# Kernel optimization log

Measured on AMD Instinct MI355X. Metric: run time of the kernel, lower is better.

## Reference

```python
import jax, jax.numpy as jnp
import numpy as np

INPUT_H = 512
INPUT_W = 512
POOL = 5
BN_EPS = 1e-5


def setup_inputs() -> dict:
    key = jax.random.key(0)
    ks = jax.random.split(key, 8)
    B = 16
    c3 = jax.random.normal(ks[0], (B, 512, 64, 64), jnp.float32)
    c4 = jax.random.normal(ks[1], (B, 1024, 32, 32), jnp.float32)
    xy = jax.random.uniform(ks[2], (B, 10, 4), jnp.float32) * 512.0
    # ensure x1<=x2, y1<=y2 like real detector boxes
    boxes = jnp.concatenate([jnp.minimum(xy[..., :2], xy[..., 2:]),
                             jnp.maximum(xy[..., :2], xy[..., 2:])], axis=-1)
    w_conv = jax.random.normal(ks[3], (512, 1536), jnp.float32) * 0.02  # 1x1 conv kernel
    b_conv = jnp.zeros((512,), jnp.float32)
    bn_gamma = jnp.ones((512,), jnp.float32)
    bn_beta = jnp.zeros((512,), jnp.float32)
    bn_mean = jax.random.normal(ks[4], (512,), jnp.float32) * 0.1
    bn_var = jax.random.uniform(ks[5], (512,), jnp.float32) * 0.5 + 0.5
    return {"c3": c3, "c4": c4, "boxes": boxes, "w_conv": w_conv, "b_conv": b_conv,
            "bn_gamma": bn_gamma, "bn_beta": bn_beta, "bn_mean": bn_mean, "bn_var": bn_var}


def _bin_weights(lo, hi, size, nout):
    """Adaptive-avg-pool bin weights over axis of length `size` for crop [lo,hi).
    Returns [nout, size] row-stochastic matrix (same math as AdaptiveAvgPool1d bins)."""
    length = hi - lo
    k = jnp.arange(nout)
    starts = lo + (k * length) // nout                      # floor(k*L/n)
    ends = lo + ((k + 1) * length + nout - 1) // nout        # ceil((k+1)*L/n)
    idx = jnp.arange(size)
    mask = (idx[None, :] >= starts[:, None]) & (idx[None, :] < ends[:, None])
    return mask.astype(jnp.float32) / (ends - starts)[:, None].astype(jnp.float32)


def reference(c3, c4, boxes, w_conv, b_conv, bn_gamma, bn_beta, bn_mean, bn_var):
    B = c3.shape[0]
    c4u = jax.image.resize(c4, (B, c4.shape[1], c4.shape[2] * 2, c4.shape[3] * 2),
                           method='bilinear')
    fused = jnp.concatenate([c3, c4u], axis=1)               # [B,1536,H,W]
    y = jnp.einsum('bchw,oc->bohw', fused, w_conv) + b_conv[None, :, None, None]
    inv = bn_gamma / jnp.sqrt(bn_var + BN_EPS)               # eval-mode BN
    y = y * inv[None, :, None, None] + (bn_beta - bn_mean * inv)[None, :, None, None]
    attr_blob = jax.nn.relu(y)                               # [B,512,H,W]
    H, W = attr_blob.shape[-2:]
    sx = W / INPUT_W
    sy = H / INPUT_H

    def pool_one(feat, box):  # feat [C,H,W], box [4] -> [C,5,5]
        x1 = jnp.clip(jnp.floor(box[0] * sx), 0, W - 1).astype(jnp.int32)
        y1 = jnp.clip(jnp.floor(box[1] * sy), 0, H - 1).astype(jnp.int32)
        x2 = jnp.clip(jnp.ceil(box[2] * sx), 0, W - 1).astype(jnp.int32)
        y2 = jnp.clip(jnp.ceil(box[3] * sy), 0, H - 1).astype(jnp.int32)
        x2 = jnp.where(x2 <= x1, jnp.minimum(x1 + 1, W), x2)
        y2 = jnp.where(y2 <= y1, jnp.minimum(y1 + 1, H), y2)
        wy = _bin_weights(y1, y2, H, POOL)                   # [5,H]
        wx = _bin_weights(x1, x2, W, POOL)                   # [5,W]
        return jnp.einsum('ph,chw,qw->cpq', wy, feat, wx)

    obj_blob = jax.vmap(lambda f, bx: jax.vmap(lambda b: pool_one(f, b))(bx))(attr_blob, boxes)
    return boxes, obj_blob  # ([B,10,4], [B,10,512,5,5])
```

## Files before the change

kernel.cpp:

```cpp
#include <hip/hip_runtime.h>
#include <stdint.h>

#define FH 64
#define FW 64
#define CIN 1536
#define C3C 512
#define C4C 1024
#define COUT 512
#define BATCH 16
#define NPIX 4096
#define NBOX 10
#define MPAD 256
#define KT128 12

typedef float v4f __attribute__((ext_vector_type(4)));
typedef long  v2l __attribute__((ext_vector_type(2)));

#define GLOAD_LDS16(g, l) __builtin_amdgcn_global_load_lds( \
    (const __attribute__((address_space(1))) void*)(g),     \
    (__attribute__((address_space(3))) void*)(l), 16, 0, 0)

#define BARRIER() asm volatile("s_barrier" ::: "memory")

__device__ __forceinline__ uint32_t pack4_fp8(float a, float b, float c, float d) {
    int lo = __builtin_amdgcn_cvt_pk_fp8_f32(a, b, 0, false);
    int v  = __builtin_amdgcn_cvt_pk_fp8_f32(c, d, lo, true);
    return (uint32_t)v;
}
__device__ __forceinline__ unsigned char f32_to_fp8(float a) {
    return (unsigned char)(__builtin_amdgcn_cvt_pk_fp8_f32(a, a, 0, false) & 0xff);
}


__global__ void prep_bn(const float* __restrict__ bng, const float* __restrict__ bnb,
                        const float* __restrict__ bnm, const float* __restrict__ bnv,
                        const float* __restrict__ bconv,
                        float* __restrict__ scale, float* __restrict__ shift) {
    int o = threadIdx.x;
    if (o < COUT) {
        float inv = bng[o] / sqrtf(bnv[o] + 1e-5f);
        scale[o] = inv * 0.0625f;
        shift[o] = bnb[o] + inv * (bconv[o] - bnm[o]);
    }
}

__global__ void conv_w(const float* __restrict__ w, unsigned char* __restrict__ w8, int n4) {
    int i = blockIdx.x * 256 + threadIdx.x;
    if (i < n4) {
        float4 f = *(const float4*)(w + i * 4);
        uint32_t v = pack4_fp8(f.x * 16.0f, f.y * 16.0f, f.z * 16.0f, f.w * 16.0f);
        int c0 = (i * 4) % CIN;
        int o  = (i * 4) / CIN;
        int k7 = c0 & 127;
        int pos = ((k7 >> 3) & 3) * 32 + (k7 >> 5) * 8 + (k7 & 7);
        *(uint32_t*)(w8 + (size_t)o * CIN + (c0 & ~127) + pos) = v;
    }
}

__global__ __launch_bounds__(256) void build_fusedT(const float* __restrict__ c3,
                                                    const float* __restrict__ c4,
                                                    unsigned char* __restrict__ fusedT) {
    __shared__ uint32_t lds[64 * 36];
    int ct = blockIdx.x;
    int y  = blockIdx.y;
    int b  = blockIdx.z;
    int t  = threadIdx.x;
    int pg = t & 15;
    int cq = t >> 4;

    #pragma unroll
    for (int r = 0; r < 2; ++r) {
        int cquad = cq + 16 * r;
        float vv[4][4];
        if (ct < 4) {
            int ch = ct * 128 + 4 * cquad;
            const float* src = c3 + (((size_t)(b * C3C + ch) * FH + y) * FW) + 4 * pg;
            #pragma unroll
            for (int k = 0; k < 4; ++k) {
                float4 f = *(const float4*)(src + (size_t)k * (FH * FW));
                vv[k][0] = f.x; vv[k][1] = f.y; vv[k][2] = f.z; vv[k][3] = f.w;
            }
        } else {
            int ch = ct * 128 - 512 + 4 * cquad;
            int jy = y >> 1;
            int jyB = min(max(jy + ((y & 1) ? 1 : -1), 0), 31);
            const float* base = c4 + (size_t)(b * C4C + ch) * 1024;
            #pragma unroll
            for (int k = 0; k < 4; ++k) {
                const float* pc = base + (size_t)k * 1024;
                float2 f0 = *(const float2*)(pc + jy * 32 + 2 * pg);
                float2 f1 = *(const float2*)(pc + jyB * 32 + 2 * pg);
                float rbA = 0.75f * f0.x + 0.25f * f1.x;
                float rbB = 0.75f * f0.y + 0.25f * f1.y;
                float rbm = __shfl_up(rbB, 1, 16);
                float rbp = __shfl_down(rbA, 1, 16);
                if (pg == 0)  rbm = rbA;
                if (pg == 15) rbp = rbB;
                vv[k][0] = 0.75f * rbA + 0.25f * rbm;
                vv[k][1] = 0.75f * rbA + 0.25f * rbB;
                vv[k][2] = 0.75f * rbB + 0.25f * rbA;
                vv[k][3] = 0.75f * rbB + 0.25f * rbp;
            }
        }
        #pragma unroll
        for (int i = 0; i < 4; ++i) {
            int px = 4 * pg + i;
            lds[px * 36 + 4 * ((cquad >> 2) ^ ((px >> 1) & 7)) + (cquad & 3)] =
                pack4_fp8(vv[0][i], vv[1][i], vv[2][i], vv[3][i]);
        }
    }
    __syncthreads();
    int g = t & 7;
    #pragma unroll
    for (int rr2 = 0; rr2 < 2; ++rr2) {
        int px = (t >> 3) + 32 * rr2;
        uint4 w = *(const uint4*)(&lds[px * 36 + 4 * (g ^ ((px >> 1) & 7))]);
        unsigned char* dst = fusedT + ((size_t)b * NPIX + y * FW + px) * CIN + ct * 128;
        int pos0 = ((2 * g) & 3) * 32 + (g >> 1) * 8;
        int pos1 = ((2 * g + 1) & 3) * 32 + (g >> 1) * 8;
        *(uint2*)(dst + pos0) = make_uint2(w.x, w.y);
        *(uint2*)(dst + pos1) = make_uint2(w.z, w.w);
    }
}

__global__ __launch_bounds__(512, 2) void gemm_bn_relu(
        const unsigned char* __restrict__ w8,
        const unsigned char* __restrict__ fusedT,
        const float* __restrict__ scale, const float* __restrict__ shift,
        unsigned char* __restrict__ attr) {
    __shared__ __align__(16) unsigned char lds_a[2][32768];
    __shared__ __align__(16) unsigned char lds_b[2][32768];
    const int t  = threadIdx.x;
    const int n0 = blockIdx.x * 256;
    const int o0 = blockIdx.y * 256;
    const int b  = blockIdx.z;
    const int wave = t >> 6, lane = t & 63;
    const int wm = wave & 1, wn = wave >> 1;
    const int quad = lane >> 4, l16 = lane & 15;
    const int cp0 = (((quad << 1) ^ (l16 & 7)) << 4);
    const int cp1 = cp0 ^ 16;
    const unsigned char* fb = fusedT + (size_t)b * NPIX * CIN;

    const int rr = t >> 3;
    const int cg = (t & 7) ^ (rr & 7);
    const unsigned char* gA = w8 + (size_t)(o0 + rr) * CIN + cg * 16;
    const unsigned char* gB = fb + (size_t)(n0 + rr) * CIN + cg * 16;

#define SA(u, kt, d) GLOAD_LDS16(gA + (size_t)(u) * (64 * CIN) + (kt) * 128, \
                                 &lds_a[d][(u) * 8192 + t * 16])
#define SB(u, kt, d) GLOAD_LDS16(gB + (size_t)(u) * (64 * CIN) + (kt) * 128, \
                                 &lds_b[d][(u) * 8192 + t * 16])
#define RAV(d, ph, i, cp) (*(const v2l*)(&lds_a[d][((wm * 128 + (ph) * 64 + (i) * 16 + l16) << 7) + (cp)]))
#define RBV(d, j, cp)     (*(const v2l*)(&lds_b[d][((wn * 64 + (j) * 16 + l16) << 7) + (cp)]))

    v4f acc[8][4];
    #pragma unroll
    for (int i = 0; i < 8; ++i)
        #pragma unroll
        for (int j = 0; j < 4; ++j) acc[i][j] = (v4f)0.0f;

    SA(0, 0, 0); SA(1, 0, 0); SA(2, 0, 0); SA(3, 0, 0);
    SB(0, 0, 0); SB(1, 0, 0); SB(2, 0, 0); SB(3, 0, 0);
    SA(0, 1, 1); SA(2, 1, 1); SB(0, 1, 1); SB(1, 1, 1); SB(2, 1, 1); SB(3, 1, 1);
    asm volatile("s_waitcnt vmcnt(6)" ::: "memory");
    BARRIER();

    v2l ah0[4], ah1[4], bh0[4], bh1[4];

    for (int kt = 0; kt < KT128; ++kt) {
        const int cur = kt & 1, nxt = cur ^ 1;

        #pragma unroll
        for (int i = 0; i < 4; ++i) { ah0[i] = RAV(cur, 0, i, cp0); ah1[i] = RAV(cur, 0, i, cp1); }
        #pragma unroll
        for (int j = 0; j < 4; ++j) { bh0[j] = RBV(cur, j, cp0); bh1[j] = RBV(cur, j, cp1); }
        if (kt > 0 && kt + 1 < KT128) {
            SA(0, kt + 1, nxt); SA(2, kt + 1, nxt);
            SB(0, kt + 1, nxt); SB(1, kt + 1, nxt);
            SB(2, kt + 1, nxt); SB(3, kt + 1, nxt);
        }
        __builtin_amdgcn_s_setprio(1);
        #pragma unroll
        for (int s = 0; s < 2; ++s)
            #pragma unroll
            for (int i = 0; i < 4; ++i)
                #pragma unroll
                for (int j = 0; j < 4; ++j)
                    acc[i][j] = __builtin_amdgcn_mfma_f32_16x16x32_fp8_fp8(ah0[i][s], bh0[j][s], acc[i][j], 0, 0, 0);
        #pragma unroll
        for (int s = 0; s < 2; ++s)
            #pragma unroll
            for (int i = 0; i < 4; ++i)
                #pragma unroll
                for (int j = 0; j < 4; ++j)
                    acc[i][j] = __builtin_amdgcn_mfma_f32_16x16x32_fp8_fp8(ah1[i][s], bh1[j][s], acc[i][j], 0, 0, 0);
        __builtin_amdgcn_s_setprio(0);
        if (kt + 1 < KT128) { asm volatile("s_waitcnt vmcnt(6)" ::: "memory"); }
        else               { asm volatile("s_waitcnt vmcnt(0)" ::: "memory"); }
        BARRIER();

        #pragma unroll
        for (int i = 0; i < 4; ++i) { ah0[i] = RAV(cur, 1, i, cp0); ah1[i] = RAV(cur, 1, i, cp1); }
        if (kt + 1 < KT128) { SA(1, kt + 1, nxt); SA(3, kt + 1, nxt); }
        __builtin_amdgcn_s_setprio(1);
        #pragma unroll
        for (int s = 0; s < 2; ++s)
            #pragma unroll
            for (int i = 0; i < 4; ++i)
                #pragma unroll
                for (int j = 0; j < 4; ++j)
                    acc[4 + i][j] = __builtin_amdgcn_mfma_f32_16x16x32_fp8_fp8(ah0[i][s], bh0[j][s], acc[4 + i][j], 0, 0, 0);
        #pragma unroll
        for (int s = 0; s < 2; ++s)
            #pragma unroll
            for (int i = 0; i < 4; ++i)
                #pragma unroll
                for (int j = 0; j < 4; ++j)
                    acc[4 + i][j] = __builtin_amdgcn_mfma_f32_16x16x32_fp8_fp8(ah1[i][s], bh1[j][s], acc[4 + i][j], 0, 0, 0);
        __builtin_amdgcn_s_setprio(0);
        if (kt + 1 < KT128) { asm volatile("s_waitcnt vmcnt(2)" ::: "memory"); }
        BARRIER();
    }

    unsigned char* ab = attr + (size_t)b * COUT * NPIX;
    #pragma unroll
    for (int a = 0; a < 8; ++a) {
        int obase = o0 + wm * 128 + (a >> 2) * 64 + (a & 3) * 16 + quad * 4;
        #pragma unroll
        for (int r = 0; r < 4; ++r) {
            int oo = obase + r;
            float sc = scale[oo], sh = shift[oo];
            #pragma unroll
            for (int j = 0; j < 4; ++j) {
                int n = n0 + wn * 64 + j * 16 + l16;
                float v = fmaxf(acc[a][j][r] * sc + sh, 0.0f);
                ab[(size_t)oo * NPIX + n] = f32_to_fp8(v);
            }
        }
    }
#undef SA
#undef SB
#undef RAV
#undef RBV
}

__global__ __launch_bounds__(256) void build_P(const float* __restrict__ boxes,
                                               unsigned char* __restrict__ P) {
    int br  = blockIdx.x;
    int m25 = blockIdx.y;
    int b   = br / NBOX;
    int m   = (br % NBOX) * 25 + m25;
    int p   = m25 / 5, q = m25 % 5;
    int t   = threadIdx.x;
    int y   = t >> 2;
    int x0  = (t & 3) * 16;
    const float* bx = boxes + (size_t)br * 4;
    int x1 = min(max((int)floorf(bx[0] * 0.125f), 0), 63);
    int y1 = min(max((int)floorf(bx[1] * 0.125f), 0), 63);
    int x2 = min(max((int)ceilf (bx[2] * 0.125f), 0), 63);
    int y2 = min(max((int)ceilf (bx[3] * 0.125f), 0), 63);
    if (x2 <= x1) x2 = min(x1 + 1, 64);
    if (y2 <= y1) y2 = min(y1 + 1, 64);
    int Lx = x2 - x1, Ly = y2 - y1;
    int sx = x1 + (q * Lx) / 5;
    int ex = x1 + ((q + 1) * Lx + 4) / 5;
    int sy = y1 + (p * Ly) / 5;
    int ey = y1 + ((p + 1) * Ly + 4) / 5;
    float wyv  = (y >= sy && y < ey) ? 1.0f / (float)(ey - sy) : 0.0f;
    float pval = 64.0f * wyv / (float)(ex - sx);
    float v[16];
    #pragma unroll
    for (int i = 0; i < 16; ++i) {
        int xi = x0 + i;
        v[i] = (xi >= sx && xi < ex) ? pval : 0.0f;
    }
    uint4 w;
    w.x = pack4_fp8(v[0],  v[1],  v[2],  v[3]);
    w.y = pack4_fp8(v[4],  v[5],  v[6],  v[7]);
    w.z = pack4_fp8(v[8],  v[9],  v[10], v[11]);
    w.w = pack4_fp8(v[12], v[13], v[14], v[15]);
    *(uint4*)(P + ((size_t)b * MPAD + m) * NPIX + y * FW + x0) = w;
}

__global__ __launch_bounds__(256) void pool_gemm(
        const unsigned char* __restrict__ P,
        const unsigned char* __restrict__ attr,
        float* __restrict__ part2) {
    __shared__ __align__(16) unsigned char lds_a[128 * 64];
    __shared__ __align__(16) unsigned char lds_b[128 * 64];
    int t  = threadIdx.x;
    int m0 = blockIdx.x * 128;
    int c0 = (blockIdx.y & 3) * 128;
    int seg = blockIdx.y >> 2;
    int b  = blockIdx.z;
    int wave = t >> 6, lane = t & 63;
    int wm = wave & 1, wn = wave >> 1;
    int quad = lane >> 4, l16 = lane & 15;
    const unsigned char* Pb = P + (size_t)b * MPAD * NPIX + seg * 1024;
    const unsigned char* ab = attr + (size_t)b * COUT * NPIX + seg * 1024;

    v4f acc[4][4];
    #pragma unroll
    for (int i = 0; i < 4; ++i)
        #pragma unroll
        for (int j = 0; j < 4; ++j) acc[i][j] = (v4f)0.0f;

    int row = t >> 2;
    int cg  = (t & 3) ^ ((row >> 1) & 3);
    const unsigned char* ga0 = Pb + (size_t)(m0 + row) * NPIX + cg * 16;
    const unsigned char* ga1 = Pb + (size_t)(m0 + row + 64) * NPIX + cg * 16;
    const unsigned char* gb0 = ab + (size_t)(c0 + row) * NPIX + cg * 16;
    const unsigned char* gb1 = ab + (size_t)(c0 + row + 64) * NPIX + cg * 16;
    unsigned char* la0 = lds_a + t * 16;
    unsigned char* la1 = lds_a + 4096 + t * 16;
    unsigned char* lb0 = lds_b + t * 16;
    unsigned char* lb1 = lds_b + 4096 + t * 16;

    int ra[4], rb[4];
    #pragma unroll
    for (int i = 0; i < 4; ++i) { ra[i] = wm * 64 + i * 16 + l16; rb[i] = wn * 64 + i * 16 + l16; }
    int q2 = quad >> 1, q1 = (quad & 1) * 8;

    for (int kt = 0; kt < 1024 / 64; ++kt) {
        __syncthreads();
        GLOAD_LDS16(ga0, la0);
        GLOAD_LDS16(ga1, la1);
        GLOAD_LDS16(gb0, lb0);
        GLOAD_LDS16(gb1, lb1);
        ga0 += 64; ga1 += 64; gb0 += 64; gb1 += 64;
        __syncthreads();

        #pragma unroll
        for (int s = 0; s < 2; ++s) {
            long af[4], bf[4];
            #pragma unroll
            for (int i = 0; i < 4; ++i) {
                int pa = (2 * s + q2) ^ ((ra[i] >> 1) & 3);
                af[i] = *(const long*)(lds_a + ra[i] * 64 + pa * 16 + q1);
                int pb = (2 * s + q2) ^ ((rb[i] >> 1) & 3);
                bf[i] = *(const long*)(lds_b + rb[i] * 64 + pb * 16 + q1);
            }
            #pragma unroll
            for (int i = 0; i < 4; ++i)
                #pragma unroll
                for (int j = 0; j < 4; ++j)
                    acc[i][j] = __builtin_amdgcn_mfma_f32_16x16x32_fp8_fp8(af[i], bf[j], acc[i][j], 0, 0, 0);
        }
    }

    float* pp = part2 + (((size_t)seg * BATCH + b) * MPAD) * COUT;
    #pragma unroll
    for (int i = 0; i < 4; ++i) {
        #pragma unroll
        for (int r = 0; r < 4; ++r) {
            int mrow = m0 + wm * 64 + i * 16 + quad * 4 + r;
            #pragma unroll
            for (int j = 0; j < 4; ++j) {
                int c = c0 + wn * 64 + j * 16 + l16;
                pp[(size_t)mrow * COUT + c] = acc[i][j][r];
            }
        }
    }
}

__global__ __launch_bounds__(256) void pool_reduce(const float* __restrict__ part2,
                                                   float* __restrict__ out) {
    const size_t SEG = (size_t)BATCH * MPAD * COUT;
    int i = blockIdx.x * 256 + threadIdx.x;
    int c = i & (COUT - 1);
    int m = (i >> 9) & (MPAD - 1);
    int b = i >> 17;
    if (m >= 250) return;
    float s = part2[i] + part2[i + SEG] + part2[i + 2 * SEG] + part2[i + 3 * SEG];
    int box = m / 25, bin = m - box * 25;
    out[640 + ((size_t)(b * NBOX + box) * COUT + c) * 25 + bin] = s * 0.015625f;
}

extern "C" void kernel_launch(void* const* d_in, const int* in_sizes, int n_in,
                              void* d_out, int out_size, void* d_ws, size_t ws_size,
                              hipStream_t stream) {
    const float* c3     = (const float*)d_in[0];
    const float* c4     = (const float*)d_in[1];
    const float* boxes  = (const float*)d_in[2];
    const float* w_conv = (const float*)d_in[3];
    const float* b_conv = (const float*)d_in[4];
    const float* bng    = (const float*)d_in[5];
    const float* bnb    = (const float*)d_in[6];
    const float* bnm    = (const float*)d_in[7];
    const float* bnv    = (const float*)d_in[8];
    float* out = (float*)d_out;

    char* ws = (char*)d_ws;
    unsigned char* fusedT = (unsigned char*)ws;
    unsigned char* P      = (unsigned char*)(ws + 100663296);
    float*         part2  = (float*)(ws + 117440512);
    unsigned char* w8     = (unsigned char*)(ws + 150994944);
    float*         scale  = (float*)(ws + 151781376);
    float*         shift  = (float*)(ws + 151783424);
    unsigned char* attr   = (unsigned char*)(ws + 151785472);

    hipMemcpyAsync(d_out, d_in[2], 640 * sizeof(float), hipMemcpyDeviceToDevice, stream);
    prep_bn<<<1, 512, 0, stream>>>(bng, bnb, bnm, bnv, b_conv, scale, shift);
    conv_w<<<(COUT * CIN / 4 + 255) / 256, 256, 0, stream>>>(w_conv, w8, COUT * CIN / 4);
    build_P<<<dim3(160, 25), 256, 0, stream>>>(boxes, P);
    build_fusedT<<<dim3(12, 64, 16), 256, 0, stream>>>(c3, c4, fusedT);
    gemm_bn_relu<<<dim3(16, 2, 16), 512, 0, stream>>>(w8, fusedT, scale, shift, attr);
    pool_gemm<<<dim3(2, 16, 16), 256, 0, stream>>>(P, attr, part2);
    pool_reduce<<<(BATCH * MPAD * COUT) / 256, 256, 0, stream>>>(part2, out);
    (void)in_sizes; (void)n_in; (void)out_size; (void)ws_size;
}
```

Baseline: 395.0 us.

## Merge prep kernels into one launch and drop split-K pooling reduce

```diff
diff --git a/kernel.cpp b/kernel.cpp
--- a/kernel.cpp
+++ b/kernel.cpp
@@ -13,6 +13,13 @@
 #define MPAD 256
 #define KT128 12
 
+#define NB_FU 12288
+#define NB_P  4000
+#define NB_W  768
+#define NB_BN 2
+#define NB_CP 3
+#define NB_TOT (NB_FU + NB_P + NB_W + NB_BN + NB_CP)
+
 typedef float v4f __attribute__((ext_vector_type(4)));
 typedef long  v2l __attribute__((ext_vector_type(2)));
 
@@ -32,94 +39,137 @@
 }
 
 
-__global__ void prep_bn(const float* __restrict__ bng, const float* __restrict__ bnb,
-                        const float* __restrict__ bnm, const float* __restrict__ bnv,
-                        const float* __restrict__ bconv,
-                        float* __restrict__ scale, float* __restrict__ shift) {
-    int o = threadIdx.x;
-    if (o < COUT) {
-        float inv = bng[o] / sqrtf(bnv[o] + 1e-5f);
-        scale[o] = inv * 0.0625f;
-        shift[o] = bnb[o] + inv * (bconv[o] - bnm[o]);
-    }
-}
-
-__global__ void conv_w(const float* __restrict__ w, unsigned char* __restrict__ w8, int n4) {
-    int i = blockIdx.x * 256 + threadIdx.x;
-    if (i < n4) {
-        float4 f = *(const float4*)(w + i * 4);
-        uint32_t v = pack4_fp8(f.x * 16.0f, f.y * 16.0f, f.z * 16.0f, f.w * 16.0f);
-        int c0 = (i * 4) % CIN;
-        int o  = (i * 4) / CIN;
-        int k7 = c0 & 127;
-        int pos = ((k7 >> 3) & 3) * 32 + (k7 >> 5) * 8 + (k7 & 7);
-        *(uint32_t*)(w8 + (size_t)o * CIN + (c0 & ~127) + pos) = v;
-    }
-}
-
-__global__ __launch_bounds__(256) void build_fusedT(const float* __restrict__ c3,
-                                                    const float* __restrict__ c4,
-                                                    unsigned char* __restrict__ fusedT) {
+__global__ __launch_bounds__(256) void mega_pre(
+        const float* __restrict__ c3, const float* __restrict__ c4,
+        const float* __restrict__ boxes,
+        const float* __restrict__ w_conv, const float* __restrict__ b_conv,
+        const float* __restrict__ bng, const float* __restrict__ bnb,
+        const float* __restrict__ bnm, const float* __restrict__ bnv,
+        unsigned char* __restrict__ fusedT, unsigned char* __restrict__ P,
+        unsigned char* __restrict__ w8,
+        float* __restrict__ scale, float* __restrict__ shift,
+        float* __restrict__ out) {
     __shared__ uint32_t lds[64 * 36];
-    int ct = blockIdx.x;
-    int y  = blockIdx.y;
-    int b  = blockIdx.z;
-    int t  = threadIdx.x;
-    int pg = t & 15;
-    int cq = t >> 4;
-
-    #pragma unroll
-    for (int r = 0; r < 2; ++r) {
-        int cquad = cq + 16 * r;
-        float vv[4][4];
-        if (ct < 4) {
-            int ch = ct * 128 + 4 * cquad;
-            const float* src = c3 + (((size_t)(b * C3C + ch) * FH + y) * FW) + 4 * pg;
-            #pragma unroll
-            for (int k = 0; k < 4; ++k) {
-                float4 f = *(const float4*)(src + (size_t)k * (FH * FW));
-                vv[k][0] = f.x; vv[k][1] = f.y; vv[k][2] = f.z; vv[k][3] = f.w;
+    const int bid = blockIdx.x;
+    const int t   = threadIdx.x;
+
+    if (bid < NB_FU) {
+        int ct = bid % 12;
+        int rest = bid / 12;
+        int y  = rest & 63;
+        int b  = rest >> 6;
+        int pg = t & 15;
+        int cq = t >> 4;
+
+        #pragma unroll
+        for (int r = 0; r < 2; ++r) {
+            int cquad = cq + 16 * r;
+            float vv[4][4];
+            if (ct < 4) {
+                int ch = ct * 128 + 4 * cquad;
+                const float* src = c3 + (((size_t)(b * C3C + ch) * FH + y) * FW) + 4 * pg;
+                #pragma unroll
+                for (int k = 0; k < 4; ++k) {
+                    float4 f = *(const float4*)(src + (size_t)k * (FH * FW));
+                    vv[k][0] = f.x; vv[k][1] = f.y; vv[k][2] = f.z; vv[k][3] = f.w;
+                }
+            } else {
+                int ch = ct * 128 - 512 + 4 * cquad;
+                int jy = y >> 1;
+                int jyB = min(max(jy + ((y & 1) ? 1 : -1), 0), 31);
+                const float* base = c4 + (size_t)(b * C4C + ch) * 1024;
+                #pragma unroll
+                for (int k = 0; k < 4; ++k) {
+                    const float* pc = base + (size_t)k * 1024;
+                    float2 f0 = *(const float2*)(pc + jy * 32 + 2 * pg);
+                    float2 f1 = *(const float2*)(pc + jyB * 32 + 2 * pg);
+                    float rbA = 0.75f * f0.x + 0.25f * f1.x;
+                    float rbB = 0.75f * f0.y + 0.25f * f1.y;
+                    float rbm = __shfl_up(rbB, 1, 16);
+                    float rbp = __shfl_down(rbA, 1, 16);
+                    if (pg == 0)  rbm = rbA;
+                    if (pg == 15) rbp = rbB;
+                    vv[k][0] = 0.75f * rbA + 0.25f * rbm;
+                    vv[k][1] = 0.75f * rbA + 0.25f * rbB;
+                    vv[k][2] = 0.75f * rbB + 0.25f * rbA;
+                    vv[k][3] = 0.75f * rbB + 0.25f * rbp;
+                }
             }
-        } else {
-            int ch = ct * 128 - 512 + 4 * cquad;
-            int jy = y >> 1;
-            int jyB = min(max(jy + ((y & 1) ? 1 : -1), 0), 31);
-            const float* base = c4 + (size_t)(b * C4C + ch) * 1024;
-            #pragma unroll
-            for (int k = 0; k < 4; ++k) {
-                const float* pc = base + (size_t)k * 1024;
-                float2 f0 = *(const float2*)(pc + jy * 32 + 2 * pg);
-                float2 f1 = *(const float2*)(pc + jyB * 32 + 2 * pg);
-                float rbA = 0.75f * f0.x + 0.25f * f1.x;
-                float rbB = 0.75f * f0.y + 0.25f * f1.y;
-                float rbm = __shfl_up(rbB, 1, 16);
-                float rbp = __shfl_down(rbA, 1, 16);
-                if (pg == 0)  rbm = rbA;
-                if (pg == 15) rbp = rbB;
-                vv[k][0] = 0.75f * rbA + 0.25f * rbm;
-                vv[k][1] = 0.75f * rbA + 0.25f * rbB;
-                vv[k][2] = 0.75f * rbB + 0.25f * rbA;
-                vv[k][3] = 0.75f * rbB + 0.25f * rbp;
+            #pragma unroll
+            for (int i = 0; i < 4; ++i) {
+                int px = 4 * pg + i;
+                lds[px * 36 + 4 * ((cquad >> 2) ^ ((px >> 1) & 7)) + (cquad & 3)] =
+                    pack4_fp8(vv[0][i], vv[1][i], vv[2][i], vv[3][i]);
             }
         }
-        #pragma unroll
-        for (int i = 0; i < 4; ++i) {
-            int px = 4 * pg + i;
-            lds[px * 36 + 4 * ((cquad >> 2) ^ ((px >> 1) & 7)) + (cquad & 3)] =
-                pack4_fp8(vv[0][i], vv[1][i], vv[2][i], vv[3][i]);
-        }
-    }
-    __syncthreads();
-    int g = t & 7;
-    #pragma unroll
-    for (int rr2 = 0; rr2 < 2; ++rr2) {
-        int px = (t >> 3) + 32 * rr2;
-        uint4 w = *(const uint4*)(&lds[px * 36 + 4 * (g ^ ((px >> 1) & 7))]);
-        unsigned char* dst = fusedT + ((size_t)b * NPIX + y * FW + px) * CIN + ct * 128;
-        int pos0 = ((2 * g) & 3) * 32 + (g >> 1) * 8;
-        int pos1 = ((2 * g + 1) & 3) * 32 + (g >> 1) * 8;
-        *(uint2*)(dst + pos0) = make_uint2(w.x, w.y);
-        *(uint2*)(dst + pos1) = make_uint2(w.z, w.w);
+        __syncthreads();
+        int g = t & 7;
+        #pragma unroll
+        for (int rr2 = 0; rr2 < 2; ++rr2) {
+            int px = (t >> 3) + 32 * rr2;
+            uint4 w = *(const uint4*)(&lds[px * 36 + 4 * (g ^ ((px >> 1) & 7))]);
+            unsigned char* dst = fusedT + ((size_t)b * NPIX + y * FW + px) * CIN + ct * 128;
+            int pos0 = ((2 * g) & 3) * 32 + (g >> 1) * 8;
+            int pos1 = ((2 * g + 1) & 3) * 32 + (g >> 1) * 8;
+            *(uint2*)(dst + pos0) = make_uint2(w.x, w.y);
+            *(uint2*)(dst + pos1) = make_uint2(w.z, w.w);
+        }
+    } else if (bid < NB_FU + NB_P) {
+        int id  = bid - NB_FU;
+        int br  = id % 160;
+        int m25 = id / 160;
+        int b   = br / NBOX;
+        int m   = (br % NBOX) * 25 + m25;
+        int p   = m25 / 5, q = m25 % 5;
+        int y   = t >> 2;
+        int x0  = (t & 3) * 16;
+        const float* bx = boxes + (size_t)br * 4;
+        int x1 = min(max((int)floorf(bx[0] * 0.125f), 0), 63);
+        int y1 = min(max((int)floorf(bx[1] * 0.125f), 0), 63);
+        int x2 = min(max((int)ceilf (bx[2] * 0.125f), 0), 63);
+        int y2 = min(max((int)ceilf (bx[3] * 0.125f), 0), 63);
+        if (x2 <= x1) x2 = min(x1 + 1, 64);
+        if (y2 <= y1) y2 = min(y1 + 1, 64);
+        int Lx = x2 - x1, Ly = y2 - y1;
+        int sx = x1 + (q * Lx) / 5;
+        int ex = x1 + ((q + 1) * Lx + 4) / 5;
+        int sy = y1 + (p * Ly) / 5;
+        int ey = y1 + ((p + 1) * Ly + 4) / 5;
+        float wyv  = (y >= sy && y < ey) ? 1.0f / (float)(ey - sy) : 0.0f;
+        float pval = 64.0f * wyv / (float)(ex - sx);
+        float v[16];
+        #pragma unroll
+        for (int i = 0; i < 16; ++i) {
+            int xi = x0 + i;
+            v[i] = (xi >= sx && xi < ex) ? pval : 0.0f;
+        }
+        uint4 w;
+        w.x = pack4_fp8(v[0],  v[1],  v[2],  v[3]);
+        w.y = pack4_fp8(v[4],  v[5],  v[6],  v[7]);
+        w.z = pack4_fp8(v[8],  v[9],  v[10], v[11]);
+        w.w = pack4_fp8(v[12], v[13], v[14], v[15]);
+        *(uint4*)(P + ((size_t)b * MPAD + m) * NPIX + y * FW + x0) = w;
+    } else if (bid < NB_FU + NB_P + NB_W) {
+        int i = (bid - NB_FU - NB_P) * 256 + t;
+        if (i < COUT * CIN / 4) {
+            float4 f = *(const float4*)(w_conv + i * 4);
+            uint32_t v = pack4_fp8(f.x * 16.0f, f.y * 16.0f, f.z * 16.0f, f.w * 16.0f);
+            int c0 = (i * 4) % CIN;
+            int o  = (i * 4) / CIN;
+            int k7 = c0 & 127;
+            int pos = ((k7 >> 3) & 3) * 32 + (k7 >> 5) * 8 + (k7 & 7);
+            *(uint32_t*)(w8 + (size_t)o * CIN + (c0 & ~127) + pos) = v;
+        }
+    } else if (bid < NB_FU + NB_P + NB_W + NB_BN) {
+        int o = (bid - NB_FU - NB_P - NB_W) * 256 + t;
+        if (o < COUT) {
+            float inv = bng[o] / sqrtf(bnv[o] + 1e-5f);
+            scale[o] = inv * 0.0625f;
+            shift[o] = bnb[o] + inv * (b_conv[o] - bnm[o]);
+        }
+    } else {
+        int i = (bid - NB_FU - NB_P - NB_W - NB_BN) * 256 + t;
+        if (i < 640) out[i] = boxes[i];
     }
 }
 
@@ -244,60 +294,21 @@
 #undef RBV
 }
 
-__global__ __launch_bounds__(256) void build_P(const float* __restrict__ boxes,
-                                               unsigned char* __restrict__ P) {
-    int br  = blockIdx.x;
-    int m25 = blockIdx.y;
-    int b   = br / NBOX;
-    int m   = (br % NBOX) * 25 + m25;
-    int p   = m25 / 5, q = m25 % 5;
-    int t   = threadIdx.x;
-    int y   = t >> 2;
-    int x0  = (t & 3) * 16;
-    const float* bx = boxes + (size_t)br * 4;
-    int x1 = min(max((int)floorf(bx[0] * 0.125f), 0), 63);
-    int y1 = min(max((int)floorf(bx[1] * 0.125f), 0), 63);
-    int x2 = min(max((int)ceilf (bx[2] * 0.125f), 0), 63);
-    int y2 = min(max((int)ceilf (bx[3] * 0.125f), 0), 63);
-    if (x2 <= x1) x2 = min(x1 + 1, 64);
-    if (y2 <= y1) y2 = min(y1 + 1, 64);
-    int Lx = x2 - x1, Ly = y2 - y1;
-    int sx = x1 + (q * Lx) / 5;
-    int ex = x1 + ((q + 1) * Lx + 4) / 5;
-    int sy = y1 + (p * Ly) / 5;
-    int ey = y1 + ((p + 1) * Ly + 4) / 5;
-    float wyv  = (y >= sy && y < ey) ? 1.0f / (float)(ey - sy) : 0.0f;
-    float pval = 64.0f * wyv / (float)(ex - sx);
-    float v[16];
-    #pragma unroll
-    for (int i = 0; i < 16; ++i) {
-        int xi = x0 + i;
-        v[i] = (xi >= sx && xi < ex) ? pval : 0.0f;
-    }
-    uint4 w;
-    w.x = pack4_fp8(v[0],  v[1],  v[2],  v[3]);
-    w.y = pack4_fp8(v[4],  v[5],  v[6],  v[7]);
-    w.z = pack4_fp8(v[8],  v[9],  v[10], v[11]);
-    w.w = pack4_fp8(v[12], v[13], v[14], v[15]);
-    *(uint4*)(P + ((size_t)b * MPAD + m) * NPIX + y * FW + x0) = w;
-}
-
-__global__ __launch_bounds__(256) void pool_gemm(
+__global__ __launch_bounds__(256) void pool_fused(
         const unsigned char* __restrict__ P,
         const unsigned char* __restrict__ attr,
-        float* __restrict__ part2) {
+        float* __restrict__ out) {
     __shared__ __align__(16) unsigned char lds_a[128 * 64];
     __shared__ __align__(16) unsigned char lds_b[128 * 64];
     int t  = threadIdx.x;
     int m0 = blockIdx.x * 128;
-    int c0 = (blockIdx.y & 3) * 128;
-    int seg = blockIdx.y >> 2;
+    int c0 = blockIdx.y * 128;
     int b  = blockIdx.z;
     int wave = t >> 6, lane = t & 63;
     int wm = wave & 1, wn = wave >> 1;
     int quad = lane >> 4, l16 = lane & 15;
-    const unsigned char* Pb = P + (size_t)b * MPAD * NPIX + seg * 1024;
-    const unsigned char* ab = attr + (size_t)b * COUT * NPIX + seg * 1024;
+    const unsigned char* Pb = P + (size_t)b * MPAD * NPIX;
+    const unsigned char* ab = attr + (size_t)b * COUT * NPIX;
 
     v4f acc[4][4];
     #pragma unroll
@@ -321,7 +332,7 @@
     for (int i = 0; i < 4; ++i) { ra[i] = wm * 64 + i * 16 + l16; rb[i] = wn * 64 + i * 16 + l16; }
     int q2 = quad >> 1, q1 = (quad & 1) * 8;
 
-    for (int kt = 0; kt < 1024 / 64; ++kt) {
+    for (int kt = 0; kt < NPIX / 64; ++kt) {
         __syncthreads();
         GLOAD_LDS16(ga0, la0);
         GLOAD_LDS16(ga1, la1);
@@ -348,32 +359,22 @@
         }
     }
 
-    float* pp = part2 + (((size_t)seg * BATCH + b) * MPAD) * COUT;
     #pragma unroll
     for (int i = 0; i < 4; ++i) {
         #pragma unroll
         for (int r = 0; r < 4; ++r) {
             int mrow = m0 + wm * 64 + i * 16 + quad * 4 + r;
-            #pragma unroll
-            for (int j = 0; j < 4; ++j) {
-                int c = c0 + wn * 64 + j * 16 + l16;
-                pp[(size_t)mrow * COUT + c] = acc[i][j][r];
+            if (mrow < 250) {
+                int box = mrow / 25, bin = mrow - box * 25;
+                float* ob = out + 640 + ((size_t)(b * NBOX + box) * COUT) * 25 + bin;
+                #pragma unroll
+                for (int j = 0; j < 4; ++j) {
+                    int c = c0 + wn * 64 + j * 16 + l16;
+                    ob[(size_t)c * 25] = acc[i][j][r] * 0.015625f;
+                }
             }
         }
     }
-}
-
-__global__ __launch_bounds__(256) void pool_reduce(const float* __restrict__ part2,
-                                                   float* __restrict__ out) {
-    const size_t SEG = (size_t)BATCH * MPAD * COUT;
-    int i = blockIdx.x * 256 + threadIdx.x;
-    int c = i & (COUT - 1);
-    int m = (i >> 9) & (MPAD - 1);
-    int b = i >> 17;
-    if (m >= 250) return;
-    float s = part2[i] + part2[i + SEG] + part2[i + 2 * SEG] + part2[i + 3 * SEG];
-    int box = m / 25, bin = m - box * 25;
-    out[640 + ((size_t)(b * NBOX + box) * COUT + c) * 25 + bin] = s * 0.015625f;
 }
 
 extern "C" void kernel_launch(void* const* d_in, const int* in_sizes, int n_in,
@@ -393,19 +394,15 @@
     char* ws = (char*)d_ws;
     unsigned char* fusedT = (unsigned char*)ws;
     unsigned char* P      = (unsigned char*)(ws + 100663296);
-    float*         part2  = (float*)(ws + 117440512);
-    unsigned char* w8     = (unsigned char*)(ws + 150994944);
-    float*         scale  = (float*)(ws + 151781376);
-    float*         shift  = (float*)(ws + 151783424);
-    unsigned char* attr   = (unsigned char*)(ws + 151785472);
-
-    hipMemcpyAsync(d_out, d_in[2], 640 * sizeof(float), hipMemcpyDeviceToDevice, stream);
-    prep_bn<<<1, 512, 0, stream>>>(bng, bnb, bnm, bnv, b_conv, scale, shift);
-    conv_w<<<(COUT * CIN / 4 + 255) / 256, 256, 0, stream>>>(w_conv, w8, COUT * CIN / 4);
-    build_P<<<dim3(160, 25), 256, 0, stream>>>(boxes, P);
-    build_fusedT<<<dim3(12, 64, 16), 256, 0, stream>>>(c3, c4, fusedT);
+    unsigned char* w8     = (unsigned char*)(ws + 117440512);
+    float*         scale  = (float*)(ws + 118226944);
+    float*         shift  = (float*)(ws + 118228992);
+    unsigned char* attr   = (unsigned char*)(ws + 118231040);
+
+    mega_pre<<<NB_TOT, 256, 0, stream>>>(c3, c4, boxes, w_conv, b_conv,
+                                         bng, bnb, bnm, bnv,
+                                         fusedT, P, w8, scale, shift, out);
     gemm_bn_relu<<<dim3(16, 2, 16), 512, 0, stream>>>(w8, fusedT, scale, shift, attr);
-    pool_gemm<<<dim3(2, 16, 16), 256, 0, stream>>>(P, attr, part2);
-    pool_reduce<<<(BATCH * MPAD * COUT) / 256, 256, 0, stream>>>(part2, out);
+    pool_fused<<<dim3(2, 4, 16), 256, 0, stream>>>(P, attr, out);
     (void)in_sizes; (void)n_in; (void)out_size; (void)ws_size;
 }
```

Result: no change. 395.5 us (+0.1%).
